# Performance work log

Measured on AMD Instinct MI355X. Metric: run time of the kernel, lower is better.

The kernel has to match this reference:

```python
import jax, jax.numpy as jnp
import numpy as np

B, D_IN, UNITS, D_OUT = 16384, 1024, 512, 512
T_END = 0.1  # ODE integrated over t in (0, 0.1)


def setup_inputs() -> dict:
    key = jax.random.key(0)
    ks = jax.random.split(key, 8)
    return {
        "x": jax.random.normal(ks[0], (B, D_IN), dtype=jnp.float32),
        "w_in": jax.random.normal(ks[1], (UNITS, D_IN), dtype=jnp.float32) * 0.02,
        "b_in": jax.random.normal(ks[2], (UNITS,), dtype=jnp.float32) * 0.02,
        "sensory_w": jax.random.normal(ks[3], (UNITS, UNITS), dtype=jnp.float32) * 0.1,
        "sensory_sigma": jax.random.normal(ks[4], (UNITS,), dtype=jnp.float32) * 0.1,
        # tau = rand(units)*0.5 + 0.5  (in [0.5, 1.0])
        "tau": jax.random.uniform(ks[5], (UNITS,), dtype=jnp.float32) * 0.5 + 0.5,
        "readout_w": jax.random.normal(ks[6], (D_OUT, UNITS), dtype=jnp.float32) * 0.02,
        "readout_b": jax.random.normal(ks[7], (D_OUT,), dtype=jnp.float32) * 0.02,
        # liquid_state buffer starts at zeros, expanded to batch
        "states": jnp.zeros((B, UNITS), dtype=jnp.float32),
    }


def reference(x, w_in, b_in, sensory_w, sensory_sigma, tau, readout_w, readout_b, states):
    # input projection: tanh(Linear(x))
    projected = jnp.tanh(x @ w_in.T + b_in)                       # [B, U]
    # sensory activation A = sigmoid(projected @ sensory_w + sigma)
    A = jax.nn.sigmoid(projected @ sensory_w + sensory_sigma)     # [B, U]
    # ODE dy/dt = (-y + A)/tau has the closed-form solution
    #   y(t) = A + (y0 - A) * exp(-t / tau)
    # which is exactly what solve_ivp(RK45) approximates at t=0.1.
    decay = jnp.exp(-T_END / tau)                                 # [U]
    new_states = A + (states - A) * decay                         # [B, U]
    # readout
    output = new_states @ readout_w.T + readout_b                 # [B, D_OUT]
    return (output, new_states)
```

## Files before the change

### kernel.cpp

```cpp
#include <hip/hip_runtime.h>
#include <stdint.h>
#include <math.h>

typedef __bf16 bf16;
typedef __bf16 bf16x8 __attribute__((ext_vector_type(8)));
typedef __bf16 bf16x4 __attribute__((ext_vector_type(4)));
typedef float f32x4 __attribute__((ext_vector_type(4)));

static constexpr int BATCH = 16384;
static constexpr int D_IN  = 1024;
static constexpr int UNITS = 512;
static constexpr int D_OUT = 512;

__device__ __forceinline__ void gll16(const void* g, void* l) {
    __builtin_amdgcn_global_load_lds(
        (const __attribute__((address_space(1))) void*)g,
        (__attribute__((address_space(3))) void*)l,
        16, 0, 0);
}

template<int N>
__device__ __forceinline__ void waitvm() {
    static_assert(N < 16, "vmcnt imm");
    __builtin_amdgcn_s_waitcnt(0x0F70 | N);
    asm volatile("" ::: "memory");
}
__device__ __forceinline__ void barrier_raw() {
    asm volatile("" ::: "memory");
    __builtin_amdgcn_s_barrier();
    asm volatile("" ::: "memory");
}

__global__ __launch_bounds__(256)
void k_prep(const float* __restrict__ w_in, const float* __restrict__ sens_w,
            const float* __restrict__ ro_w,
            bf16* __restrict__ w_in_bf, bf16* __restrict__ sensT, bf16* __restrict__ ro_bf)
{
    __shared__ float tile[32][33];
    const int b = blockIdx.x;
    const int t = threadIdx.x;
    if (b < 512) {
        int i = b * 256 + t;
        f32x4 v = ((const f32x4*)w_in)[i];
        bf16x4 o = { (bf16)v.x, (bf16)v.y, (bf16)v.z, (bf16)v.w };
        ((bf16x4*)w_in_bf)[i] = o;
    } else if (b < 768) {
        int bb = b - 512;
        int bx = bb & 15, by = bb >> 4;
        int tx = t & 31, ty = t >> 5;
        #pragma unroll
        for (int j = ty; j < 32; j += 8)
            tile[j][tx] = sens_w[(size_t)(by * 32 + j) * UNITS + bx * 32 + tx];
        __syncthreads();
        #pragma unroll
        for (int j = ty; j < 32; j += 8)
            sensT[(size_t)(bx * 32 + j) * UNITS + by * 32 + tx] = (bf16)tile[tx][j];
    } else {
        int i = (b - 768) * 256 + t;
        f32x4 v = ((const f32x4*)ro_w)[i];
        bf16x4 o = { (bf16)v.x, (bf16)v.y, (bf16)v.z, (bf16)v.w };
        ((bf16x4*)ro_bf)[i] = o;
    }
}

template<int K, int EPI, bool AF32, int DEPTH>
__global__ __launch_bounds__(256, 4)
void k_gemm(const float* __restrict__ Af, const bf16* __restrict__ Ab,
            const bf16* __restrict__ Bw,
            const float* __restrict__ bias,
            const float* __restrict__ tau,
            const float* __restrict__ states,
            float* __restrict__ outF, bf16* __restrict__ outB,
            int M, int N)
{
    constexpr int NSTEP = K / 32;
    constexpr int L = AF32 ? 4 : 3;
    constexpr int ABPB = AF32 ? 8192 : 4096;
    __shared__ __align__(16) char sAraw[DEPTH][ABPB];
    __shared__ __align__(16) char sBraw[DEPTH][8192];

    const int t = threadIdx.x;
    const int ntiles = N >> 7;
    const int nwg = gridDim.x;
    const int d = blockIdx.x;
    const int bid = (d & 7) * (nwg >> 3) + (d >> 3);
    const int mtile = bid / ntiles;
    const int ntile = bid % ntiles;
    const int m0 = mtile << 6, n0 = ntile << 7;

    const int lane = t & 63;
    const int wave = t >> 6;
    const int wr = (wave >> 1) * 32;
    const int wc = (wave & 1) * 64;
    const int l15 = lane & 15;
    const int lk  = (lane >> 4) * 8;

    f32x4 acc[2][4];
    #pragma unroll
    for (int m = 0; m < 2; ++m)
        #pragma unroll
        for (int n = 0; n < 4; ++n)
            acc[m][n] = (f32x4){0.f, 0.f, 0.f, 0.f};

    const int brow = t >> 2;
    const int bslot = ((t & 3) ^ ((brow >> 1) & 3)) * 16;
    const char* bsrc = (const char*)Bw + (size_t)(n0 + brow) * K * 2 + bslot;
    const char* asrcb = AF32 ? nullptr
                             : ((const char*)Ab + (size_t)(m0 + brow) * K * 2 + bslot);
    const int ar = t >> 3;
    const int aslot = ((t & 7) ^ (ar & 7)) * 16;
    const char* asrcf = AF32 ? ((const char*)Af + (size_t)(m0 + ar) * K * 4 + aslot)
                             : nullptr;

    auto STAGE = [&](int buf, int kt) {
        if constexpr (AF32) {
            const size_t kb = (size_t)kt * 4;
            gll16(asrcf + kb,                      &sAraw[buf][t * 16]);
            gll16(asrcf + kb + (size_t)32 * K * 4, &sAraw[buf][4096 + t * 16]);
        } else {
            gll16(asrcb + (size_t)kt * 2, &sAraw[buf][t * 16]);
        }
        const size_t kb2 = (size_t)kt * 2;
        gll16(bsrc + kb2,                      &sBraw[buf][t * 16]);
        gll16(bsrc + kb2 + (size_t)64 * K * 2, &sBraw[buf][4096 + t * 16]);
    };

    const int Rb = wc + l15;
    const int boff = Rb * 64 + ((lk * 2) ^ (((Rb >> 1) & 3) << 4));
    const int Ra = wr + l15;
    int aoff0, aoff1 = 0;
    if constexpr (AF32) {
        const int s = (Ra & 7) << 4;
        aoff0 = Ra * 128 + ((lk * 4) ^ s);
        aoff1 = Ra * 128 + ((lk * 4 + 16) ^ s);
    } else {
        aoff0 = Ra * 64 + ((lk * 2) ^ (((Ra >> 1) & 3) << 4));
    }

    auto COMPUTE = [&](int buf) {
        const char* aB = sAraw[buf];
        const char* bB = sBraw[buf];
        bf16x8 afr[2], bfr[4];
        #pragma unroll
        for (int m = 0; m < 2; ++m) {
            if constexpr (AF32) {
                f32x4 h0 = *(const f32x4*)(aB + aoff0 + m * 2048);
                f32x4 h1 = *(const f32x4*)(aB + aoff1 + m * 2048);
                afr[m] = (bf16x8){ (bf16)h0.x, (bf16)h0.y, (bf16)h0.z, (bf16)h0.w,
                                   (bf16)h1.x, (bf16)h1.y, (bf16)h1.z, (bf16)h1.w };
            } else {
                afr[m] = *(const bf16x8*)(aB + aoff0 + m * 1024);
            }
        }
        #pragma unroll
        for (int n = 0; n < 4; ++n)
            bfr[n] = *(const bf16x8*)(bB + boff + n * 1024);
        #pragma unroll
        for (int m = 0; m < 2; ++m)
            #pragma unroll
            for (int n = 0; n < 4; ++n)
                acc[m][n] = __builtin_amdgcn_mfma_f32_16x16x32_bf16(
                                afr[m], bfr[n], acc[m][n], 0, 0, 0);
    };

    #pragma unroll
    for (int p = 0; p < DEPTH; ++p) STAGE(p, p * 32);

    int buf = 0;
    int kt_stage = DEPTH * 32;
    for (int i = 0; i < NSTEP - (DEPTH - 1); ++i) {
        waitvm<(DEPTH - 1) * L>();
        barrier_raw();
        COMPUTE(buf);
        barrier_raw();
        if (kt_stage < K) { STAGE(buf, kt_stage); kt_stage += 32; }
        buf = (buf + 1 == DEPTH) ? 0 : buf + 1;
    }
    if constexpr (DEPTH == 3) {
        waitvm<L>(); barrier_raw(); COMPUTE(buf);
        buf = (buf + 1 == DEPTH) ? 0 : buf + 1;
    }
    waitvm<0>(); barrier_raw(); COMPUTE(buf);
    asm volatile("" ::: "memory");

    const int rbase = m0 + wr + ((lane >> 4) << 2);
    const int cbase = n0 + wc + l15;
    #pragma unroll
    for (int n = 0; n < 4; ++n) {
        const int gc = cbase + n * 16;
        const float bv = bias[gc];
        float dec = 0.f;
        if constexpr (EPI == 2) dec = __expf(-0.1f / tau[gc]);
        #pragma unroll
        for (int m = 0; m < 2; ++m) {
            #pragma unroll
            for (int r = 0; r < 4; ++r) {
                const int gr = rbase + m * 16 + r;
                float v = acc[m][n][r] + bv;
                if constexpr (EPI == 1) {
                    float tv = 1.0f - 2.0f / (1.0f + __expf(2.0f * v));
                    outB[(size_t)gr * N + gc] = (bf16)tv;
                } else if constexpr (EPI == 2) {
                    float a = 1.0f / (1.0f + __expf(-v));
                    float s = states[(size_t)gr * N + gc];
                    outF[(size_t)gr * N + gc] = a + (s - a) * dec;
                } else {
                    outF[(size_t)gr * N + gc] = v;
                }
            }
        }
    }
}

extern "C" void kernel_launch(void* const* d_in, const int* in_sizes, int n_in,
                              void* d_out, int out_size, void* d_ws, size_t ws_size,
                              hipStream_t stream) {
    const float* x        = (const float*)d_in[0];
    const float* w_in     = (const float*)d_in[1];
    const float* b_in     = (const float*)d_in[2];
    const float* sens_w   = (const float*)d_in[3];
    const float* sens_sig = (const float*)d_in[4];
    const float* tau      = (const float*)d_in[5];
    const float* ro_w     = (const float*)d_in[6];
    const float* ro_b     = (const float*)d_in[7];
    const float* states   = (const float*)d_in[8];

    float* out    = (float*)d_out;
    float* new_st = out + (size_t)BATCH * D_OUT;
    bf16*  proj   = (bf16*)d_out;

    bf16* w_in_bf = (bf16*)d_ws;
    bf16* sensT   = w_in_bf + (size_t)UNITS * D_IN;
    bf16* ro_bf   = sensT + (size_t)UNITS * UNITS;

    k_prep<<<1024, 256, 0, stream>>>(w_in, sens_w, ro_w, w_in_bf, sensT, ro_bf);

    k_gemm<1024, 1, true, 2><<<(BATCH / 64) * (UNITS / 128), 256, 0, stream>>>(
        x, nullptr, w_in_bf, b_in, nullptr, nullptr, nullptr, proj, BATCH, UNITS);

    k_gemm<512, 2, false, 3><<<(BATCH / 64) * (UNITS / 128), 256, 0, stream>>>(
        nullptr, proj, sensT, sens_sig, tau, states, new_st, nullptr, BATCH, UNITS);

    k_gemm<512, 3, true, 2><<<(BATCH / 64) * (D_OUT / 128), 256, 0, stream>>>(
        new_st, nullptr, ro_bf, ro_b, nullptr, nullptr, out, nullptr, BATCH, D_OUT);
}
```

Baseline: 87.62 us.

## Use full-width N tiles for fp32-A GEMMs and 128x128 tiles for middle GEMM

```diff
diff --git a/kernel.cpp b/kernel.cpp
--- a/kernel.cpp
+++ b/kernel.cpp
@@ -63,102 +63,79 @@
     }
 }
 
-template<int K, int EPI, bool AF32, int DEPTH>
-__global__ __launch_bounds__(256, 4)
-void k_gemm(const float* __restrict__ Af, const bf16* __restrict__ Ab,
-            const bf16* __restrict__ Bw,
-            const float* __restrict__ bias,
-            const float* __restrict__ tau,
-            const float* __restrict__ states,
-            float* __restrict__ outF, bf16* __restrict__ outB,
-            int M, int N)
+template<int K, int EPI>
+__global__ __launch_bounds__(512, 2)
+void k_gwide(const float* __restrict__ Af, const bf16* __restrict__ Bw,
+             const float* __restrict__ bias,
+             float* __restrict__ outF, bf16* __restrict__ outB, int M)
 {
+    constexpr int N = 512;
     constexpr int NSTEP = K / 32;
-    constexpr int L = AF32 ? 4 : 3;
-    constexpr int ABPB = AF32 ? 8192 : 4096;
-    __shared__ __align__(16) char sAraw[DEPTH][ABPB];
-    __shared__ __align__(16) char sBraw[DEPTH][8192];
+    constexpr int DEPTH = 3, L = 5;
+    __shared__ __align__(16) char sA[DEPTH][8192];
+    __shared__ __align__(16) char sB[DEPTH][32768];
 
     const int t = threadIdx.x;
-    const int ntiles = N >> 7;
     const int nwg = gridDim.x;
     const int d = blockIdx.x;
     const int bid = (d & 7) * (nwg >> 3) + (d >> 3);
-    const int mtile = bid / ntiles;
-    const int ntile = bid % ntiles;
-    const int m0 = mtile << 6, n0 = ntile << 7;
+    const int m0 = bid << 6;
 
     const int lane = t & 63;
     const int wave = t >> 6;
-    const int wr = (wave >> 1) * 32;
-    const int wc = (wave & 1) * 64;
+    const int wr = (wave >> 2) * 32;
+    const int wc = (wave & 3) * 128;
     const int l15 = lane & 15;
     const int lk  = (lane >> 4) * 8;
 
-    f32x4 acc[2][4];
+    f32x4 acc[2][8];
     #pragma unroll
     for (int m = 0; m < 2; ++m)
         #pragma unroll
-        for (int n = 0; n < 4; ++n)
+        for (int n = 0; n < 8; ++n)
             acc[m][n] = (f32x4){0.f, 0.f, 0.f, 0.f};
 
-    const int brow = t >> 2;
-    const int bslot = ((t & 3) ^ ((brow >> 1) & 3)) * 16;
-    const char* bsrc = (const char*)Bw + (size_t)(n0 + brow) * K * 2 + bslot;
-    const char* asrcb = AF32 ? nullptr
-                             : ((const char*)Ab + (size_t)(m0 + brow) * K * 2 + bslot);
     const int ar = t >> 3;
     const int aslot = ((t & 7) ^ (ar & 7)) * 16;
-    const char* asrcf = AF32 ? ((const char*)Af + (size_t)(m0 + ar) * K * 4 + aslot)
-                             : nullptr;
+    const char* asrc = (const char*)Af + (size_t)(m0 + ar) * K * 4 + aslot;
+    const int br = t >> 2;
+    const int bslot = ((t & 3) ^ ((br >> 1) & 3)) * 16;
+    const char* bsrc = (const char*)Bw + (size_t)br * K * 2 + bslot;
 
     auto STAGE = [&](int buf, int kt) {
-        if constexpr (AF32) {
-            const size_t kb = (size_t)kt * 4;
-            gll16(asrcf + kb,                      &sAraw[buf][t * 16]);
-            gll16(asrcf + kb + (size_t)32 * K * 4, &sAraw[buf][4096 + t * 16]);
-        } else {
-            gll16(asrcb + (size_t)kt * 2, &sAraw[buf][t * 16]);
-        }
-        const size_t kb2 = (size_t)kt * 2;
-        gll16(bsrc + kb2,                      &sBraw[buf][t * 16]);
-        gll16(bsrc + kb2 + (size_t)64 * K * 2, &sBraw[buf][4096 + t * 16]);
+        gll16(asrc + (size_t)kt * 4, &sA[buf][t * 16]);
+        const size_t kb = (size_t)kt * 2;
+        gll16(bsrc + kb,                        &sB[buf][t * 16]);
+        gll16(bsrc + kb + (size_t)128 * K * 2,  &sB[buf][8192  + t * 16]);
+        gll16(bsrc + kb + (size_t)256 * K * 2,  &sB[buf][16384 + t * 16]);
+        gll16(bsrc + kb + (size_t)384 * K * 2,  &sB[buf][24576 + t * 16]);
     };
 
+    const int Ra = wr + l15;
+    const int sa = (Ra & 7) << 4;
+    const int aoff0 = Ra * 128 + ((lk * 4) ^ sa);
+    const int aoff1 = Ra * 128 + ((lk * 4 + 16) ^ sa);
     const int Rb = wc + l15;
     const int boff = Rb * 64 + ((lk * 2) ^ (((Rb >> 1) & 3) << 4));
-    const int Ra = wr + l15;
-    int aoff0, aoff1 = 0;
-    if constexpr (AF32) {
-        const int s = (Ra & 7) << 4;
-        aoff0 = Ra * 128 + ((lk * 4) ^ s);
-        aoff1 = Ra * 128 + ((lk * 4 + 16) ^ s);
-    } else {
-        aoff0 = Ra * 64 + ((lk * 2) ^ (((Ra >> 1) & 3) << 4));
-    }
 
     auto COMPUTE = [&](int buf) {
-        const char* aB = sAraw[buf];
-        const char* bB = sBraw[buf];
-        bf16x8 afr[2], bfr[4];
+        const char* aB = sA[buf];
+        const char* bB = sB[buf];
+        bf16x8 afr[2], bfr[8];
         #pragma unroll
         for (int m = 0; m < 2; ++m) {
-            if constexpr (AF32) {
-                f32x4 h0 = *(const f32x4*)(aB + aoff0 + m * 2048);
-                f32x4 h1 = *(const f32x4*)(aB + aoff1 + m * 2048);
-                afr[m] = (bf16x8){ (bf16)h0.x, (bf16)h0.y, (bf16)h0.z, (bf16)h0.w,
-                                   (bf16)h1.x, (bf16)h1.y, (bf16)h1.z, (bf16)h1.w };
-            } else {
-                afr[m] = *(const bf16x8*)(aB + aoff0 + m * 1024);
-            }
+            f32x4 h0 = *(const f32x4*)(aB + aoff0 + m * 2048);
+            f32x4 h1 = *(const f32x4*)(aB + aoff1 + m * 2048);
+            afr[m] = (bf16x8){ (bf16)h0.x, (bf16)h0.y, (bf16)h0.z, (bf16)h0.w,
+                               (bf16)h1.x, (bf16)h1.y, (bf16)h1.z, (bf16)h1.w };
         }
         #pragma unroll
-        for (int n = 0; n < 4; ++n)
+        for (int n = 0; n < 8; ++n)
             bfr[n] = *(const bf16x8*)(bB + boff + n * 1024);
         #pragma unroll
         for (int m = 0; m < 2; ++m)
             #pragma unroll
-            for (int n = 0; n < 4; ++n)
+            for (int n = 0; n < 8; ++n)
                 acc[m][n] = __builtin_amdgcn_mfma_f32_16x16x32_bf16(
                                 afr[m], bfr[n], acc[m][n], 0, 0, 0);
     };
@@ -176,21 +153,17 @@
         if (kt_stage < K) { STAGE(buf, kt_stage); kt_stage += 32; }
         buf = (buf + 1 == DEPTH) ? 0 : buf + 1;
     }
-    if constexpr (DEPTH == 3) {
-        waitvm<L>(); barrier_raw(); COMPUTE(buf);
-        buf = (buf + 1 == DEPTH) ? 0 : buf + 1;
-    }
+    waitvm<L>(); barrier_raw(); COMPUTE(buf);
+    buf = (buf + 1 == DEPTH) ? 0 : buf + 1;
     waitvm<0>(); barrier_raw(); COMPUTE(buf);
     asm volatile("" ::: "memory");
 
     const int rbase = m0 + wr + ((lane >> 4) << 2);
-    const int cbase = n0 + wc + l15;
-    #pragma unroll
-    for (int n = 0; n < 4; ++n) {
+    const int cbase = wc + l15;
+    #pragma unroll
+    for (int n = 0; n < 8; ++n) {
         const int gc = cbase + n * 16;
         const float bv = bias[gc];
-        float dec = 0.f;
-        if constexpr (EPI == 2) dec = __expf(-0.1f / tau[gc]);
         #pragma unroll
         for (int m = 0; m < 2; ++m) {
             #pragma unroll
@@ -200,13 +173,117 @@
                 if constexpr (EPI == 1) {
                     float tv = 1.0f - 2.0f / (1.0f + __expf(2.0f * v));
                     outB[(size_t)gr * N + gc] = (bf16)tv;
-                } else if constexpr (EPI == 2) {
-                    float a = 1.0f / (1.0f + __expf(-v));
-                    float s = states[(size_t)gr * N + gc];
-                    outF[(size_t)gr * N + gc] = a + (s - a) * dec;
                 } else {
                     outF[(size_t)gr * N + gc] = v;
                 }
+            }
+        }
+    }
+}
+
+template<int K, int EPI>
+__global__ __launch_bounds__(512, 4)
+void k_gemm8(const bf16* __restrict__ Ab, const bf16* __restrict__ Bw,
+             const float* __restrict__ bias,
+             const float* __restrict__ tau, const float* __restrict__ states,
+             float* __restrict__ outF, int M, int N)
+{
+    constexpr int NSTEP = K / 32;
+    constexpr int DEPTH = 3, L = 2;
+    __shared__ __align__(16) char sA[DEPTH][8192];
+    __shared__ __align__(16) char sB[DEPTH][8192];
+
+    const int t = threadIdx.x;
+    const int ntiles = N >> 7;
+    const int nwg = gridDim.x;
+    const int d = blockIdx.x;
+    const int bid = (d & 7) * (nwg >> 3) + (d >> 3);
+    const int mtile = bid / ntiles;
+    const int ntile = bid % ntiles;
+    const int m0 = mtile << 7, n0 = ntile << 7;
+
+    const int lane = t & 63;
+    const int wave = t >> 6;
+    const int wr = (wave >> 1) * 32;
+    const int wc = (wave & 1) * 64;
+    const int l15 = lane & 15;
+    const int lk  = (lane >> 4) * 8;
+
+    f32x4 acc[2][4];
+    #pragma unroll
+    for (int m = 0; m < 2; ++m)
+        #pragma unroll
+        for (int n = 0; n < 4; ++n)
+            acc[m][n] = (f32x4){0.f, 0.f, 0.f, 0.f};
+
+    const int row = t >> 2;
+    const int slot = ((t & 3) ^ ((row >> 1) & 3)) * 16;
+    const char* asrc = (const char*)Ab + (size_t)(m0 + row) * K * 2 + slot;
+    const char* bsrc = (const char*)Bw + (size_t)(n0 + row) * K * 2 + slot;
+
+    auto STAGE = [&](int buf, int kt) {
+        const size_t kb = (size_t)kt * 2;
+        gll16(asrc + kb, &sA[buf][t * 16]);
+        gll16(bsrc + kb, &sB[buf][t * 16]);
+    };
+
+    const int Ra = wr + l15;
+    const int aoff = Ra * 64 + ((lk * 2) ^ (((Ra >> 1) & 3) << 4));
+    const int Rb = wc + l15;
+    const int boff = Rb * 64 + ((lk * 2) ^ (((Rb >> 1) & 3) << 4));
+
+    auto COMPUTE = [&](int buf) {
+        const char* aB = sA[buf];
+        const char* bB = sB[buf];
+        bf16x8 afr[2], bfr[4];
+        #pragma unroll
+        for (int m = 0; m < 2; ++m)
+            afr[m] = *(const bf16x8*)(aB + aoff + m * 1024);
+        #pragma unroll
+        for (int n = 0; n < 4; ++n)
+            bfr[n] = *(const bf16x8*)(bB + boff + n * 1024);
+        #pragma unroll
+        for (int m = 0; m < 2; ++m)
+            #pragma unroll
+            for (int n = 0; n < 4; ++n)
+                acc[m][n] = __builtin_amdgcn_mfma_f32_16x16x32_bf16(
+                                afr[m], bfr[n], acc[m][n], 0, 0, 0);
+    };
+
+    #pragma unroll
+    for (int p = 0; p < DEPTH; ++p) STAGE(p, p * 32);
+
+    int buf = 0;
+    int kt_stage = DEPTH * 32;
+    for (int i = 0; i < NSTEP - (DEPTH - 1); ++i) {
+        waitvm<(DEPTH - 1) * L>();
+        barrier_raw();
+        COMPUTE(buf);
+        barrier_raw();
+        if (kt_stage < K) { STAGE(buf, kt_stage); kt_stage += 32; }
+        buf = (buf + 1 == DEPTH) ? 0 : buf + 1;
+    }
+    waitvm<L>(); barrier_raw(); COMPUTE(buf);
+    buf = (buf + 1 == DEPTH) ? 0 : buf + 1;
+    waitvm<0>(); barrier_raw(); COMPUTE(buf);
+    asm volatile("" ::: "memory");
+
+    const int rbase = m0 + wr + ((lane >> 4) << 2);
+    const int cbase = n0 + wc + l15;
+    #pragma unroll
+    for (int n = 0; n < 4; ++n) {
+        const int gc = cbase + n * 16;
+        const float bv = bias[gc];
+        const float dec = __expf(-0.1f / tau[gc]);
+        #pragma unroll
+        for (int m = 0; m < 2; ++m) {
+            #pragma unroll
+            for (int r = 0; r < 4; ++r) {
+                const int gr = rbase + m * 16 + r;
+                float v = acc[m][n][r] + bv;
+                float a = 1.0f / (1.0f + __expf(-v));
+                float s = states[(size_t)gr * N + gc];
+                outF[(size_t)gr * N + gc] = a + (s - a) * dec;
             }
         }
     }
@@ -235,12 +312,12 @@
 
     k_prep<<<1024, 256, 0, stream>>>(w_in, sens_w, ro_w, w_in_bf, sensT, ro_bf);
 
-    k_gemm<1024, 1, true, 2><<<(BATCH / 64) * (UNITS / 128), 256, 0, stream>>>(
-        x, nullptr, w_in_bf, b_in, nullptr, nullptr, nullptr, proj, BATCH, UNITS);
-
-    k_gemm<512, 2, false, 3><<<(BATCH / 64) * (UNITS / 128), 256, 0, stream>>>(
-        nullptr, proj, sensT, sens_sig, tau, states, new_st, nullptr, BATCH, UNITS);
-
-    k_gemm<512, 3, true, 2><<<(BATCH / 64) * (D_OUT / 128), 256, 0, stream>>>(
-        new_st, nullptr, ro_bf, ro_b, nullptr, nullptr, out, nullptr, BATCH, D_OUT);
-}
+    k_gwide<1024, 1><<<BATCH / 64, 512, 0, stream>>>(
+        x, w_in_bf, b_in, nullptr, proj, BATCH);
+
+    k_gemm8<512, 2><<<(BATCH / 128) * (UNITS / 128), 512, 0, stream>>>(
+        proj, sensT, sens_sig, tau, states, new_st, BATCH, UNITS);
+
+    k_gwide<512, 3><<<BATCH / 64, 512, 0, stream>>>(
+        new_st, ro_bf, ro_b, out, nullptr, BATCH);
+}
```

Result: slower. 93.74 us (+7.0%).
